# Performance work log

Measured on AMD Instinct MI355X. Metric: run time of the kernel, lower is better.

The kernel has to match this reference:

```python
import jax, jax.numpy as jnp
import numpy as np

B, T, C = 8, 2048, 1024
NEG_INF = -1e38


def setup_inputs() -> dict:
    key = jax.random.key(0)
    ks = jax.random.split(key, 10)
    s = 1.0 / np.sqrt(C)
    return {
        "x": jax.random.normal(ks[0], (B, T, C), jnp.float32),
        "Wk": jax.random.normal(ks[1], (C, C), jnp.float32) * s,
        "Wv": jax.random.normal(ks[2], (C, C), jnp.float32) * s,
        "Wr": jax.random.normal(ks[3], (C, C), jnp.float32) * s,
        "Wo": jax.random.normal(ks[4], (C, C), jnp.float32) * s,
        "time_decay": jax.random.normal(ks[5], (C,), jnp.float32) * 0.5,
        "time_first": jax.random.normal(ks[6], (C,), jnp.float32) * 0.5,
        "time_mix_key": jax.random.uniform(ks[7], (1, 1, C), jnp.float32),
        "time_mix_value": jax.random.uniform(ks[8], (1, 1, C), jnp.float32),
        "time_mix_receptance": jax.random.uniform(ks[9], (1, 1, C), jnp.float32),
    }


def _wkv(k, v, time_decay, time_first):
    # k, v: [B, T, C]; numerically-stabilized exp-sum recurrence over T
    w = -jnp.exp(time_decay)  # [C]
    u = time_first            # [C]

    def step(carry, kv):
        num, den, mx = carry
        kt, vt = kv  # [B, C]
        # output at this step uses u bonus
        m_out = jnp.maximum(mx, kt + u)
        e1 = jnp.exp(mx - m_out)
        e2 = jnp.exp(kt + u - m_out)
        out = (e1 * num + e2 * vt) / (e1 * den + e2)
        # state update with decay w
        m_new = jnp.maximum(mx + w, kt)
        e1 = jnp.exp(mx + w - m_new)
        e2 = jnp.exp(kt - m_new)
        return (e1 * num + e2 * vt, e1 * den + e2, m_new), out

    init = (jnp.zeros((B, C), jnp.float32),
            jnp.zeros((B, C), jnp.float32),
            jnp.full((B, C), NEG_INF, jnp.float32))
    kT = jnp.swapaxes(k, 0, 1)  # [T, B, C]
    vT = jnp.swapaxes(v, 0, 1)
    _, outs = jax.lax.scan(step, init, (kT, vT))
    return jnp.swapaxes(outs, 0, 1)  # [B, T, C]


def reference(x, Wk, Wv, Wr, Wo, time_decay, time_first,
              time_mix_key, time_mix_value, time_mix_receptance):
    # time_shift: prev_x[t] = x[t-1], zero at t=0
    prev_x = jnp.concatenate([jnp.zeros_like(x[:, :1]), x[:, :-1]], axis=1)

    r_in = x * time_mix_receptance + prev_x * (1 - time_mix_receptance)
    k_in = x * time_mix_key + prev_x * (1 - time_mix_key)
    v_in = x * time_mix_value + prev_x * (1 - time_mix_value)

    receptance = jnp.einsum('btc,dc->btd', r_in, Wr)
    key = jnp.einsum('btc,dc->btd', k_in, Wk)
    value = jnp.einsum('btc,dc->btd', v_in, Wv)

    wkv = _wkv(key, value, time_decay, time_first)
    rwkv = jax.nn.sigmoid(receptance) * wkv
    return jnp.einsum('btc,dc->btd', rwkv, Wo)
```

## Files before the change

kernel.cpp:

```cpp
#include <hip/hip_runtime.h>
#include <cstdint>
#include <cstddef>

#define DEVI __device__ __forceinline__

typedef __attribute__((ext_vector_type(8))) short short8;
typedef __attribute__((ext_vector_type(4))) float f32x4;

constexpr int Bc = 8, Tc = 2048, Cc = 1024;
constexpr int WKV_L = 32, WKV_NCH = 64;

DEVI unsigned short f2b(float f) {
  unsigned int u = __float_as_uint(f);
  unsigned int r = (u + 0x7FFFu + ((u >> 16) & 1u)) >> 16;
  return (unsigned short)r;
}
DEVI float b2f(unsigned short u) {
  return __uint_as_float(((unsigned int)u) << 16);
}

DEVI void gload16(const unsigned short* g, unsigned short* l) {
  __builtin_amdgcn_global_load_lds(
      (const __attribute__((address_space(1))) void*)g,
      (__attribute__((address_space(3))) void*)l, 16, 0, 0);
}

#define FENCE() asm volatile("" ::: "memory")

__global__ void convert4_kernel(const float* __restrict__ W0,
                                const float* __restrict__ W1,
                                const float* __restrict__ W2,
                                const float* __restrict__ W3,
                                unsigned short* __restrict__ o0,
                                unsigned short* __restrict__ o1,
                                unsigned short* __restrict__ o2,
                                unsigned short* __restrict__ o3) {
  const int i = blockIdx.x * blockDim.x + threadIdx.x;
  const int s = blockIdx.y;
  const float* in = s == 0 ? W0 : (s == 1 ? W1 : (s == 2 ? W2 : W3));
  unsigned short* out = s == 0 ? o0 : (s == 1 ? o1 : (s == 2 ? o2 : o3));
  const float4 v = ((const float4*)in)[i];
  ushort4 o;
  o.x = f2b(v.x); o.y = f2b(v.y); o.z = f2b(v.z); o.w = f2b(v.w);
  ((ushort4*)out)[i] = o;
}

__global__ void mix3_kernel(const float* __restrict__ x,
                            const float* __restrict__ tmk,
                            const float* __restrict__ tmv,
                            const float* __restrict__ tmr,
                            unsigned short* __restrict__ kin,
                            unsigned short* __restrict__ vin,
                            unsigned short* __restrict__ rin,
                            long n4) {
  long i = (long)blockIdx.x * blockDim.x + threadIdx.x;
  const long stride = (long)gridDim.x * blockDim.x;
  for (; i < n4; i += stride) {
    const long e = i * 4;
    const int c = (int)(e & (Cc - 1));
    const long bt = e >> 10;
    const int t = (int)(bt & (Tc - 1));
    const float4 xv = *(const float4*)(x + e);
    float4 pv = {0.f, 0.f, 0.f, 0.f};
    if (t > 0) pv = *(const float4*)(x + e - Cc);
    const float4 mk = *(const float4*)(tmk + c);
    const float4 mv = *(const float4*)(tmv + c);
    const float4 mr = *(const float4*)(tmr + c);
    const float* xp = (const float*)&xv;
    const float* pp = (const float*)&pv;
    const float* mkp = (const float*)&mk;
    const float* mvp = (const float*)&mv;
    const float* mrp = (const float*)&mr;
    ushort4 ko, vo, ro;
    unsigned short* kop = (unsigned short*)&ko;
    unsigned short* vop = (unsigned short*)&vo;
    unsigned short* rop = (unsigned short*)&ro;
#pragma unroll
    for (int q = 0; q < 4; ++q) {
      kop[q] = f2b(xp[q] * mkp[q] + pp[q] * (1.f - mkp[q]));
      vop[q] = f2b(xp[q] * mvp[q] + pp[q] * (1.f - mvp[q]));
      rop[q] = f2b(xp[q] * mrp[q] + pp[q] * (1.f - mrp[q]));
    }
    *(ushort4*)(kin + e) = ko;
    *(ushort4*)(vin + e) = vo;
    *(ushort4*)(rin + e) = ro;
  }
}

template <typename OutT>
__global__ __launch_bounds__(512, 2)
void gemm256(const unsigned short* __restrict__ A0,
             const unsigned short* __restrict__ W0, OutT* __restrict__ C0,
             const unsigned short* __restrict__ A1,
             const unsigned short* __restrict__ W1, OutT* __restrict__ C1,
             const unsigned short* __restrict__ A2,
             const unsigned short* __restrict__ W2, OutT* __restrict__ C2,
             int K, int N) {
  constexpr int BK = 64;
  __shared__ alignas(16) unsigned short As[2][256 * BK];
  __shared__ alignas(16) unsigned short Bs[2][256 * BK];
  const int z = blockIdx.z;
  const unsigned short* A = z == 0 ? A0 : (z == 1 ? A1 : A2);
  const unsigned short* W = z == 0 ? W0 : (z == 1 ? W1 : W2);
  OutT* C_out = z == 0 ? C0 : (z == 1 ? C1 : C2);
  const int h = (int)blockIdx.x + ((int)blockIdx.y << 6);
  const int m0 = ((((h & 7) << 3) | ((h >> 3) & 7))) << 8;
  const int n0 = (h >> 6) << 8;
  const int tid = threadIdx.x;
  const int lane = tid & 63;
  const int w = tid >> 6;
  const int wm = w >> 2;
  const int wn = w & 3;
  const int fr = lane & 15;
  const int ksl = lane >> 4;

  f32x4 acc[8][4];
#pragma unroll
  for (int i = 0; i < 8; ++i)
#pragma unroll
    for (int j = 0; j < 4; ++j) acc[i][j] = (f32x4){0.f, 0.f, 0.f, 0.f};

#define STAGE(buf, kt)                                                        \
  {                                                                           \
    _Pragma("unroll")                                                         \
    for (int cc = 0; cc < 4; ++cc) {                                          \
      const int c = w * 256 + cc * 64 + lane;                                 \
      const int row = c >> 3;                                                 \
      const int gsl = (c & 7) ^ (row & 7);                                    \
      gload16(A + (size_t)(m0 + row) * K + (kt) + gsl * 8,                    \
              &As[buf][(w * 256 + cc * 64) * 8]);                             \
      gload16(W + (size_t)(n0 + row) * K + (kt) + gsl * 8,                    \
              &Bs[buf][(w * 256 + cc * 64) * 8]);                             \
    }                                                                         \
  }

#define LDSRD(bufp, row, sl) \
  (*(const short8*)&(bufp)[(row) * 64 + ((((sl) ^ ((row) & 7))) * 8)])

  const int nt = K / BK;
  STAGE(0, 0);
  int cur = 0;
  for (int t = 0; t < nt; ++t) {
    asm volatile("s_waitcnt vmcnt(0)" ::: "memory");
    __builtin_amdgcn_s_barrier();
    FENCE();
    if (t + 1 < nt) STAGE(cur ^ 1, (t + 1) * BK);
    const unsigned short* Ab = As[cur];
    const unsigned short* Bb = Bs[cur];
    const int sl0 = ksl;
    const int sl1 = 4 + ksl;
    short8 a0[4], b0[4], a1g[4], a2g[4], b2[4], a3[4];
#pragma unroll
    for (int i = 0; i < 4; ++i)
      a0[i] = LDSRD(Ab, wm * 128 + i * 16 + fr, sl0);
#pragma unroll
    for (int j = 0; j < 4; ++j)
      b0[j] = LDSRD(Bb, wn * 64 + j * 16 + fr, sl0);
#pragma unroll
    for (int i = 0; i < 4; ++i)
      a1g[i] = LDSRD(Ab, wm * 128 + (4 + i) * 16 + fr, sl0);
#pragma unroll
    for (int i = 0; i < 4; ++i)
#pragma unroll
      for (int j = 0; j < 4; ++j)
        acc[i][j] = __builtin_amdgcn_mfma_f32_16x16x32_bf16(a0[i], b0[j],
                                                            acc[i][j], 0, 0, 0);
#pragma unroll
    for (int i = 0; i < 4; ++i)
      a2g[i] = LDSRD(Ab, wm * 128 + i * 16 + fr, sl1);
#pragma unroll
    for (int j = 0; j < 4; ++j)
      b2[j] = LDSRD(Bb, wn * 64 + j * 16 + fr, sl1);
#pragma unroll
    for (int i = 0; i < 4; ++i)
#pragma unroll
      for (int j = 0; j < 4; ++j)
        acc[4 + i][j] = __builtin_amdgcn_mfma_f32_16x16x32_bf16(a1g[i], b0[j],
                                                                acc[4 + i][j], 0, 0, 0);
#pragma unroll
    for (int i = 0; i < 4; ++i)
      a3[i] = LDSRD(Ab, wm * 128 + (4 + i) * 16 + fr, sl1);
#pragma unroll
    for (int i = 0; i < 4; ++i)
#pragma unroll
      for (int j = 0; j < 4; ++j)
        acc[i][j] = __builtin_amdgcn_mfma_f32_16x16x32_bf16(a2g[i], b2[j],
                                                            acc[i][j], 0, 0, 0);
#pragma unroll
    for (int i = 0; i < 4; ++i)
#pragma unroll
      for (int j = 0; j < 4; ++j)
        acc[4 + i][j] = __builtin_amdgcn_mfma_f32_16x16x32_bf16(a3[i], b2[j],
                                                                acc[4 + i][j], 0, 0, 0);
    FENCE();
    cur ^= 1;
  }
#undef STAGE
#undef LDSRD

  const int orow = (lane >> 4) * 4;
  const int ocol = lane & 15;
#pragma unroll
  for (int i = 0; i < 8; ++i)
#pragma unroll
    for (int j = 0; j < 4; ++j) {
      const size_t rbase = (size_t)(m0 + wm * 128 + i * 16 + orow);
      const int cb = n0 + wn * 64 + j * 16 + ocol;
#pragma unroll
      for (int q = 0; q < 4; ++q) {
        const float vq = acc[i][j][q];
        if constexpr (sizeof(OutT) == 2)
          C_out[(rbase + q) * N + cb] = (OutT)f2b(vq);
        else
          C_out[(rbase + q) * N + cb] = (OutT)vq;
      }
    }
}

__global__ void wkv_phase1(const unsigned short* __restrict__ keyb,
                           const unsigned short* __restrict__ valb,
                           const float* __restrict__ td,
                           float* __restrict__ s_num,
                           float* __restrict__ s_den,
                           float* __restrict__ s_mx) {
  const int g = blockIdx.x * blockDim.x + threadIdx.x;
  const int c = g & (Cc - 1);
  const int j = (g / Cc) & (WKV_NCH - 1);
  const int b = g / (Cc * WKV_NCH);
  const float w = -__expf(td[c]);
  float num = 0.f, den = 0.f, mx = -1e38f;
  size_t idx = ((size_t)b * Tc + (size_t)j * WKV_L) * Cc + c;
#pragma unroll 4
  for (int i = 0; i < WKV_L; ++i, idx += Cc) {
    const float kt = b2f(keyb[idx]);
    const float vt = b2f(valb[idx]);
    const float mw = mx + w;
    const bool cg = mw >= kt;
    const float d = __expf(cg ? kt - mw : mw - kt);
    const float a1 = cg ? 1.f : d;
    const float a2 = cg ? d : 1.f;
    num = a1 * num + a2 * vt;
    den = a1 * den + a2;
    mx = cg ? mw : kt;
  }
  s_num[g] = num; s_den[g] = den; s_mx[g] = mx;
}

__global__ void wkv_phase2(const float* __restrict__ td,
                           float* __restrict__ s_num,
                           float* __restrict__ s_den,
                           float* __restrict__ s_mx) {
  const int g = blockIdx.x * blockDim.x + threadIdx.x;
  const int c = g & (Cc - 1);
  const int b = g / Cc;
  const float Lw = -__expf(td[c]) * (float)WKV_L;
  float num = 0.f, den = 0.f, mx = -1e38f;
  size_t base = (size_t)b * WKV_NCH * Cc + c;
  for (int j = 0; j < WKV_NCH; ++j) {
    const size_t s = base + (size_t)j * Cc;
    const float ln = s_num[s], ld = s_den[s], lm = s_mx[s];
    s_num[s] = num; s_den[s] = den; s_mx[s] = mx;
    const float md = mx + Lw;
    const bool cg = md >= lm;
    const float d = __expf(cg ? lm - md : md - lm);
    const float e1 = cg ? 1.f : d;
    const float e2 = cg ? d : 1.f;
    num = e1 * num + e2 * ln;
    den = e1 * den + e2 * ld;
    mx = cg ? md : lm;
  }
}

__global__ void wkv_phase3(const unsigned short* __restrict__ keyb,
                           const unsigned short* __restrict__ valb,
                           const unsigned short* __restrict__ recb,
                           const float* __restrict__ td,
                           const float* __restrict__ tf,
                           const float* __restrict__ s_num,
                           const float* __restrict__ s_den,
                           const float* __restrict__ s_mx,
                           unsigned short* __restrict__ rwkv) {
  const int g = blockIdx.x * blockDim.x + threadIdx.x;
  const int c = g & (Cc - 1);
  const int j = (g / Cc) & (WKV_NCH - 1);
  const int b = g / (Cc * WKV_NCH);
  const float w = -__expf(td[c]);
  const float u = tf[c];
  float num = s_num[g], den = s_den[g], mx = s_mx[g];
  size_t idx = ((size_t)b * Tc + (size_t)j * WKV_L) * Cc + c;
#pragma unroll 2
  for (int i = 0; i < WKV_L; ++i, idx += Cc) {
    const float kt = b2f(keyb[idx]);
    const float vt = b2f(valb[idx]);
    const float rt = b2f(recb[idx]);
    const float ku = kt + u;
    const bool co = mx >= ku;
    const float dd = __expf(co ? ku - mx : mx - ku);
    const float e1 = co ? 1.f : dd;
    const float e2 = co ? dd : 1.f;
    const float out = (e1 * num + e2 * vt) / (e1 * den + e2);
    const float sr = 1.f / (1.f + __expf(-rt));
    rwkv[idx] = f2b(sr * out);
    const float mw = mx + w;
    const bool cg = mw >= kt;
    const float du = __expf(cg ? kt - mw : mw - kt);
    const float a1 = cg ? 1.f : du;
    const float a2 = cg ? du : 1.f;
    num = a1 * num + a2 * vt;
    den = a1 * den + a2;
    mx = cg ? mw : kt;
  }
}

extern "C" void kernel_launch(void* const* d_in, const int* in_sizes, int n_in,
                              void* d_out, int out_size, void* d_ws, size_t ws_size,
                              hipStream_t stream) {
  const float* x   = (const float*)d_in[0];
  const float* Wk  = (const float*)d_in[1];
  const float* Wv  = (const float*)d_in[2];
  const float* Wr  = (const float*)d_in[3];
  const float* Wo  = (const float*)d_in[4];
  const float* td  = (const float*)d_in[5];
  const float* tf  = (const float*)d_in[6];
  const float* tmk = (const float*)d_in[7];
  const float* tmv = (const float*)d_in[8];
  const float* tmr = (const float*)d_in[9];

  const long BT = (long)Bc * Tc;
  const long NE = BT * Cc;
  const long CC = (long)Cc * Cc;

  char* p = (char*)d_ws;
  unsigned short* Wk_b = (unsigned short*)p; p += CC * 2;
  unsigned short* Wv_b = (unsigned short*)p; p += CC * 2;
  unsigned short* Wr_b = (unsigned short*)p; p += CC * 2;
  unsigned short* Wo_b = (unsigned short*)p; p += CC * 2;
  unsigned short* kin  = (unsigned short*)p; p += NE * 2;
  unsigned short* vin  = (unsigned short*)p; p += NE * 2;
  unsigned short* rin  = (unsigned short*)p; p += NE * 2;
  unsigned short* keyb = (unsigned short*)p; p += NE * 2;
  unsigned short* valb = (unsigned short*)p; p += NE * 2;
  unsigned short* recb = (unsigned short*)p; p += NE * 2;
  unsigned short* rwkv = kin;
  const long NS = (long)Bc * WKV_NCH * Cc;
  float* s_num = (float*)vin;
  float* s_den = s_num + NS;
  float* s_mx  = s_den + NS;

  {
    dim3 g((unsigned)(CC / 4 / 256), 4), b_(256);
    convert4_kernel<<<g, b_, 0, stream>>>(Wk, Wv, Wr, Wo,
                                          Wk_b, Wv_b, Wr_b, Wo_b);
  }

  mix3_kernel<<<2048, 256, 0, stream>>>(x, tmk, tmv, tmr, kin, vin, rin, NE / 4);

  {
    dim3 grid((unsigned)(BT / 256), (unsigned)(Cc / 256), 3), blk(512);
    gemm256<unsigned short><<<grid, blk, 0, stream>>>(
        kin, Wk_b, keyb, vin, Wv_b, valb, rin, Wr_b, recb, Cc, Cc);
  }

  wkv_phase1<<<2048, 256, 0, stream>>>(keyb, valb, td, s_num, s_den, s_mx);
  wkv_phase2<<<32, 256, 0, stream>>>(td, s_num, s_den, s_mx);
  wkv_phase3<<<2048, 256, 0, stream>>>(keyb, valb, recb, td, tf,
                                       s_num, s_den, s_mx, rwkv);

  {
    dim3 grid((unsigned)(BT / 256), (unsigned)(Cc / 256), 1), blk(512);
    gemm256<float><<<grid, blk, 0, stream>>>(
        rwkv, Wo_b, (float*)d_out, rwkv, Wo_b, (float*)d_out,
        rwkv, Wo_b, (float*)d_out, Cc, Cc);
  }
}
```

Measured before the change: 263.5 us.

## Interleave next-tile global loads with MFMA phases and add setprio in GEMM

Restructures the GEMM main loop into four phases. Each phase issues a slice of the next tile's global-to-LDS loads, waits on a partial vmcnt, passes a barrier, then runs 16 MFMAs. The intent is to spread memory traffic across the compute so loads overlap MFMA work instead of being issued in one burst and fully drained at the top of each iteration. MFMA blocks are also wrapped in s_setprio to favour matrix issue. The cost is many more block barriers per K-step and a fragile vmcnt-based ordering.

```diff
diff --git a/kernel.cpp b/kernel.cpp
--- a/kernel.cpp
+++ b/kernel.cpp
@@ -89,13 +89,13 @@
 
 template <typename OutT>
 __global__ __launch_bounds__(512, 2)
-void gemm256(const unsigned short* __restrict__ A0,
-             const unsigned short* __restrict__ W0, OutT* __restrict__ C0,
-             const unsigned short* __restrict__ A1,
-             const unsigned short* __restrict__ W1, OutT* __restrict__ C1,
-             const unsigned short* __restrict__ A2,
-             const unsigned short* __restrict__ W2, OutT* __restrict__ C2,
-             int K, int N) {
+void gemm256e(const unsigned short* __restrict__ A0,
+              const unsigned short* __restrict__ W0, OutT* __restrict__ C0,
+              const unsigned short* __restrict__ A1,
+              const unsigned short* __restrict__ W1, OutT* __restrict__ C1,
+              const unsigned short* __restrict__ A2,
+              const unsigned short* __restrict__ W2, OutT* __restrict__ C2,
+              int K, int N) {
   constexpr int BK = 64;
   __shared__ alignas(16) unsigned short As[2][256 * BK];
   __shared__ alignas(16) unsigned short Bs[2][256 * BK];
@@ -113,6 +113,9 @@
   const int wn = w & 3;
   const int fr = lane & 15;
   const int ksl = lane >> 4;
+  const int gb = wn >> 1;
+  const int rb = (wm << 1) | (wn & 1);
+  const int ra = wn;
 
   f32x4 acc[8][4];
 #pragma unroll
@@ -120,83 +123,128 @@
 #pragma unroll
     for (int j = 0; j < 4; ++j) acc[i][j] = (f32x4){0.f, 0.f, 0.f, 0.f};
 
-#define STAGE(buf, kt)                                                        \
+#define STA(buf, kt, r)                                                       \
   {                                                                           \
-    _Pragma("unroll")                                                         \
-    for (int cc = 0; cc < 4; ++cc) {                                          \
-      const int c = w * 256 + cc * 64 + lane;                                 \
-      const int row = c >> 3;                                                 \
-      const int gsl = (c & 7) ^ (row & 7);                                    \
-      gload16(A + (size_t)(m0 + row) * K + (kt) + gsl * 8,                    \
-              &As[buf][(w * 256 + cc * 64) * 8]);                             \
-      gload16(W + (size_t)(n0 + row) * K + (kt) + gsl * 8,                    \
-              &Bs[buf][(w * 256 + cc * 64) * 8]);                             \
-    }                                                                         \
+    const int bc = (r) * 8;                                                   \
+    const int c = bc + lane;                                                  \
+    const int row = c >> 3;                                                   \
+    const int gsl = (c & 7) ^ (row & 7);                                      \
+    gload16(A + (size_t)(m0 + row) * K + (kt) + gsl * 8, &As[buf][bc * 8]);   \
+  }
+#define STB(buf, kt, r)                                                       \
+  {                                                                           \
+    const int bc = (r) * 8;                                                   \
+    const int c = bc + lane;                                                  \
+    const int row = c >> 3;                                                   \
+    const int gsl = (c & 7) ^ (row & 7);                                      \
+    gload16(W + (size_t)(n0 + row) * K + (kt) + gsl * 8, &Bs[buf][bc * 8]);   \
   }
 
 #define LDSRD(bufp, row, sl) \
   (*(const short8*)&(bufp)[(row) * 64 + ((((sl) ^ ((row) & 7))) * 8)])
 
+#define MFMA16(ar, bi, br)                                                    \
+  {                                                                           \
+    __builtin_amdgcn_s_setprio(1);                                            \
+    _Pragma("unroll")                                                         \
+    for (int i = 0; i < 4; ++i)                                               \
+      _Pragma("unroll")                                                       \
+      for (int j = 0; j < 4; ++j)                                             \
+        acc[(bi) + i][j] = __builtin_amdgcn_mfma_f32_16x16x32_bf16(           \
+            ar[i], br[j], acc[(bi) + i][j], 0, 0, 0);                         \
+    __builtin_amdgcn_s_setprio(0);                                            \
+  }
+
   const int nt = K / BK;
-  STAGE(0, 0);
-  int cur = 0;
+#pragma unroll
+  for (int cc = 0; cc < 4; ++cc) {
+    const int r = (w * 256 + cc * 64) >> 3;
+    STA(0, 0, r);
+    STB(0, 0, r);
+  }
+  asm volatile("s_waitcnt vmcnt(0)" ::: "memory");
+  __builtin_amdgcn_s_barrier();
+  FENCE();
+
   for (int t = 0; t < nt; ++t) {
-    asm volatile("s_waitcnt vmcnt(0)" ::: "memory");
-    __builtin_amdgcn_s_barrier();
-    FENCE();
-    if (t + 1 < nt) STAGE(cur ^ 1, (t + 1) * BK);
+    const int cur = t & 1, nb = cur ^ 1;
+    const int kt1 = (t + 1) * BK;
+    const bool st = (t + 1 < nt);
     const unsigned short* Ab = As[cur];
     const unsigned short* Bb = Bs[cur];
-    const int sl0 = ksl;
-    const int sl1 = 4 + ksl;
-    short8 a0[4], b0[4], a1g[4], a2g[4], b2[4], a3[4];
+    const int sl0 = ksl, sl1 = 4 + ksl;
+    short8 af[4], bf[4];
 #pragma unroll
     for (int i = 0; i < 4; ++i)
-      a0[i] = LDSRD(Ab, wm * 128 + i * 16 + fr, sl0);
+      af[i] = LDSRD(Ab, wm * 128 + i * 16 + fr, sl0);
 #pragma unroll
     for (int j = 0; j < 4; ++j)
-      b0[j] = LDSRD(Bb, wn * 64 + j * 16 + fr, sl0);
+      bf[j] = LDSRD(Bb, wn * 64 + j * 16 + fr, sl0);
+    if (st) {
+      STB(nb, kt1, gb * 128 + rb * 16 + 0);
+      STB(nb, kt1, gb * 128 + rb * 16 + 8);
+      asm volatile("s_waitcnt vmcnt(4)" ::: "memory");
+    } else {
+      asm volatile("s_waitcnt vmcnt(2)" ::: "memory");
+    }
+    __builtin_amdgcn_s_barrier();
+    FENCE();
+    MFMA16(af, 0, bf);
+    FENCE();
+    __builtin_amdgcn_s_barrier();
 #pragma unroll
     for (int i = 0; i < 4; ++i)
-      a1g[i] = LDSRD(Ab, wm * 128 + (4 + i) * 16 + fr, sl0);
+      af[i] = LDSRD(Ab, wm * 128 + (4 + i) * 16 + fr, sl0);
+    if (st) {
+      STB(nb, kt1, gb * 128 + 64 + rb * 16 + 0);
+      STB(nb, kt1, gb * 128 + 64 + rb * 16 + 8);
+      asm volatile("s_waitcnt vmcnt(4)" ::: "memory");
+    } else {
+      asm volatile("s_waitcnt vmcnt(0)" ::: "memory");
+    }
+    __builtin_amdgcn_s_barrier();
+    FENCE();
+    MFMA16(af, 4, bf);
+    FENCE();
+    __builtin_amdgcn_s_barrier();
 #pragma unroll
     for (int i = 0; i < 4; ++i)
-#pragma unroll
-      for (int j = 0; j < 4; ++j)
-        acc[i][j] = __builtin_amdgcn_mfma_f32_16x16x32_bf16(a0[i], b0[j],
-                                                            acc[i][j], 0, 0, 0);
+      af[i] = LDSRD(Ab, wm * 128 + i * 16 + fr, sl1);
+#pragma unroll
+    for (int j = 0; j < 4; ++j)
+      bf[j] = LDSRD(Bb, wn * 64 + j * 16 + fr, sl1);
+    if (st) {
+      STA(nb, kt1, wm * 128 + ra * 16 + 0);
+      STA(nb, kt1, wm * 128 + ra * 16 + 8);
+      asm volatile("s_waitcnt vmcnt(4)" ::: "memory");
+    } else {
+      asm volatile("s_waitcnt vmcnt(0)" ::: "memory");
+    }
+    __builtin_amdgcn_s_barrier();
+    FENCE();
+    MFMA16(af, 0, bf);
+    FENCE();
+    __builtin_amdgcn_s_barrier();
 #pragma unroll
     for (int i = 0; i < 4; ++i)
-      a2g[i] = LDSRD(Ab, wm * 128 + i * 16 + fr, sl1);
-#pragma unroll
-    for (int j = 0; j < 4; ++j)
-      b2[j] = LDSRD(Bb, wn * 64 + j * 16 + fr, sl1);
-#pragma unroll
-    for (int i = 0; i < 4; ++i)
-#pragma unroll
-      for (int j = 0; j < 4; ++j)
-        acc[4 + i][j] = __builtin_amdgcn_mfma_f32_16x16x32_bf16(a1g[i], b0[j],
-                                                                acc[4 + i][j], 0, 0, 0);
-#pragma unroll
-    for (int i = 0; i < 4; ++i)
-      a3[i] = LDSRD(Ab, wm * 128 + (4 + i) * 16 + fr, sl1);
-#pragma unroll
-    for (int i = 0; i < 4; ++i)
-#pragma unroll
-      for (int j = 0; j < 4; ++j)
-        acc[i][j] = __builtin_amdgcn_mfma_f32_16x16x32_bf16(a2g[i], b2[j],
-                                                            acc[i][j], 0, 0, 0);
-#pragma unroll
-    for (int i = 0; i < 4; ++i)
-#pragma unroll
-      for (int j = 0; j < 4; ++j)
-        acc[4 + i][j] = __builtin_amdgcn_mfma_f32_16x16x32_bf16(a3[i], b2[j],
-                                                                acc[4 + i][j], 0, 0, 0);
-    FENCE();
-    cur ^= 1;
-  }
-#undef STAGE
+      af[i] = LDSRD(Ab, wm * 128 + (4 + i) * 16 + fr, sl1);
+    if (st) {
+      STA(nb, kt1, wm * 128 + 64 + ra * 16 + 0);
+      STA(nb, kt1, wm * 128 + 64 + ra * 16 + 8);
+      asm volatile("s_waitcnt vmcnt(4)" ::: "memory");
+    } else {
+      asm volatile("s_waitcnt vmcnt(0)" ::: "memory");
+    }
+    __builtin_amdgcn_s_barrier();
+    FENCE();
+    MFMA16(af, 4, bf);
+    FENCE();
+    __builtin_amdgcn_s_barrier();
+  }
+#undef STA
+#undef STB
 #undef LDSRD
+#undef MFMA16
 
   const int orow = (lane >> 4) * 4;
   const int ocol = lane & 15;
@@ -357,7 +405,7 @@
 
   {
     dim3 grid((unsigned)(BT / 256), (unsigned)(Cc / 256), 3), blk(512);
-    gemm256<unsigned short><<<grid, blk, 0, stream>>>(
+    gemm256e<unsigned short><<<grid, blk, 0, stream>>>(
         kin, Wk_b, keyb, vin, Wv_b, valb, rin, Wr_b, recb, Cc, Cc);
   }
 
@@ -368,7 +416,7 @@
 
   {
     dim3 grid((unsigned)(BT / 256), (unsigned)(Cc / 256), 1), blk(512);
-    gemm256<float><<<grid, blk, 0, stream>>>(
+    gemm256e<float><<<grid, blk, 0, stream>>>(
         rwkv, Wo_b, (float*)d_out, rwkv, Wo_b, (float*)d_out,
         rwkv, Wo_b, (float*)d_out, Cc, Cc);
   }
```

After: 258.6 us (median of 2 runs). Within noise of the previous version (-1.9%).
